# Performance work log

Measured on AMD Instinct MI355X. Metric: run time of the kernel, lower is better.

The kernel has to match this reference:

```python
import jax, jax.numpy as jnp
import numpy as np

# ---- Plane / hashgrid static configuration (matches init_kwargs + gridencoder defaults) ----
LEVEL_DIM = 2
NUM_LEVELS = 16
LOG2_HASHMAP = 19
HASHMAP_MAX = 2 ** LOG2_HASHMAP
BASE_RES = 16               # gridencoder default base_resolution
RESOLUTION = 2048           # desired_resolution
OUTPUT_DIM = 8
HIDDEN_DIM = 64
N_POINTS = 1 << 20
PRIME_Y = np.uint32(2654435761)  # torch-ngp fast_hash prime for dim 1 (dim 0 prime is 1)

# per-level scales / resolutions / table offsets, exactly as in gridencoder
_b = np.exp2(np.log2(RESOLUTION / BASE_RES) / (NUM_LEVELS - 1))
SCALES, RESOLUTIONS, OFFSETS = [], [], [0]
for _l in range(NUM_LEVELS):
    _s = BASE_RES * (_b ** _l) - 1.0
    _r = int(np.ceil(_s)) + 1
    SCALES.append(float(_s)); RESOLUTIONS.append(_r)
    _p = min(HASHMAP_MAX, _r * _r)
    _p = (_p + 7) // 8 * 8  # align to 8 entries
    OFFSETS.append(OFFSETS[-1] + _p)
TOTAL_PARAMS = OFFSETS[-1]


def grid_encode(x, table):
    """Multires 2D hashgrid encoding. x: [N,2] in [0,1], table: [TOTAL_PARAMS, LEVEL_DIM]."""
    feats = []
    for l in range(NUM_LEVELS):
        scale, res = SCALES[l], RESOLUTIONS[l]
        size = OFFSETS[l + 1] - OFFSETS[l]
        pos = x * scale + 0.5                 # [N,2]
        pg = jnp.floor(pos)
        fr = pos - pg                         # bilinear fractions within grid cell
        pg = pg.astype(jnp.uint32)
        acc = jnp.zeros((x.shape[0], LEVEL_DIM), x.dtype)
        for dx in (0, 1):
            for dy in (0, 1):
                gx = pg[:, 0] + jnp.uint32(dx)
                gy = pg[:, 1] + jnp.uint32(dy)
                if res * res > size:
                    # hashed level: fast_hash (xor of prime-multiplied coords) mod table size
                    idx = (gx ^ (gy * PRIME_Y)) % jnp.uint32(size)
                else:
                    # dense level: row-major index, wrapped like the CUDA kernel
                    idx = (gx + gy * jnp.uint32(res)) % jnp.uint32(size)
                wx = fr[:, 0] if dx else 1.0 - fr[:, 0]
                wy = fr[:, 1] if dy else 1.0 - fr[:, 1]
                acc = acc + (wx * wy)[:, None] * table[OFFSETS[l] + idx.astype(jnp.int32)]
        feats.append(acc)
    return jnp.concatenate(feats, axis=-1)  # [N, NUM_LEVELS*LEVEL_DIM] = [N, 32]


def mlp(h, w0, w1):
    # 2-layer bias-free MLP: Linear(32->64) + relu + Linear(64->8)
    return jax.nn.relu(h @ w0.T) @ w1.T


def plane_forward(xy, table, w0, w1, bound):
    xy = (xy + bound) / (2 * bound)
    coords = jnp.clip(xy * RESOLUTION - 0.5, 0, RESOLUTION - 1)
    cx, cy = coords[..., 0], coords[..., 1]
    cx0, cy0 = jnp.floor(cx), jnp.floor(cy)
    cx1 = jnp.clip(cx0 + 1, 0, RESOLUTION - 1)
    cy1 = jnp.clip(cy0 + 1, 0, RESOLUTION - 1)
    u = (cx - cx0)[..., None]
    v = (cy - cy0)[..., None]

    def corner(a, b):
        g = (jnp.stack([a, b], axis=-1) + 0.5) / RESOLUTION
        return mlp(grid_encode(g, table), w0, w1)

    f00 = corner(cx0, cy0)
    f01 = corner(cx0, cy1)
    f10 = corner(cx1, cy0)
    f11 = corner(cx1, cy1)
    return (1 - v) * (1 - u) * f00 + (1 - v) * u * f10 + v * (1 - u) * f01 + v * u * f11


def setup_inputs() -> dict:
    key = jax.random.key(0)
    k1, k2, k3, k4 = jax.random.split(key, 4)
    xy = jax.random.normal(k1, (N_POINTS, 2), jnp.float32)
    table = jax.random.uniform(k2, (TOTAL_PARAMS, LEVEL_DIM), jnp.float32, -1e-4, 1e-4)
    in_dim = NUM_LEVELS * LEVEL_DIM
    w0 = jax.random.normal(k3, (HIDDEN_DIM, in_dim), jnp.float32) * (1.0 / np.sqrt(in_dim))
    w1 = jax.random.normal(k4, (OUTPUT_DIM, HIDDEN_DIM), jnp.float32) * (1.0 / np.sqrt(HIDDEN_DIM))
    return {"xy": xy, "table": table, "w0": w0, "w1": w1, "bound": 1}


def reference(xy, table, w0, w1, bound):
    return plane_forward(xy, table, w0, w1, bound)
```

## Files before the change

### kernel.cpp

```cpp
#include <hip/hip_runtime.h>
#include <math.h>

#define PRIME_Y 2654435761u

struct LevelParams { float scale; unsigned res; unsigned size; unsigned offset; };
struct EncParams { LevelParams lv[16]; };

typedef __attribute__((ext_vector_type(8))) short short8;
typedef __attribute__((ext_vector_type(4))) float f32x4;

struct alignas(8) F2 { float x, y; };

__device__ inline unsigned bf2pack(float a, float b) {
  unsigned r;
  asm("v_cvt_pk_bf16_f32 %0, %1, %2" : "=v"(r) : "v"(a), "v"(b));
  return r;
}
__device__ inline F2 bf2unpack(unsigned u) {
  F2 r;
  r.x = __uint_as_float(u << 16);
  r.y = __uint_as_float(u & 0xFFFF0000u);
  return r;
}

__global__ __launch_bounds__(256) void cvt_table(const F2* __restrict__ in,
                                                 unsigned* __restrict__ outb,
                                                 int n) {
  int i = blockIdx.x * 256 + threadIdx.x;
  if (i < n) {
    F2 v = in[i];
    outb[i] = bf2pack(v.x, v.y);
  }
}

__global__ __launch_bounds__(256) void prep_tables(
    const F2* __restrict__ in, unsigned long long* __restrict__ pair,
    unsigned* __restrict__ packed, EncParams P, unsigned denseTotal,
    unsigned total) {
  unsigned i = blockIdx.x * 256 + threadIdx.x;
  if (i >= total) return;
  F2 a = in[i];
  unsigned pa = bf2pack(a.x, a.y);
  if (i >= denseTotal) { packed[i] = pa; return; }
  unsigned off = 0, size = 0;
  #pragma unroll
  for (int l = 0; l < 12; ++l)
    if (i >= P.lv[l].offset) { off = P.lv[l].offset; size = P.lv[l].size; }
  unsigned j = i - off;
  unsigned j1 = (j + 1u == size) ? 0u : (j + 1u);
  F2 b = in[off + j1];
  pair[i] = ((unsigned long long)bf2pack(b.x, b.y) << 32) | (unsigned long long)pa;
}

#define SMEM_BYTES 39936

template <int TBF>
__global__ __launch_bounds__(256, 4) void plane_fwd(
    const F2* __restrict__ xy,
    const F2* __restrict__ table,
    const unsigned* __restrict__ tbf16,
    const unsigned long long* __restrict__ dpair,
    const float* __restrict__ w0g,
    const float* __restrict__ w1g,
    const int* __restrict__ boundp,
    float* __restrict__ out,
    EncParams P)
{
  __shared__ __align__(16) char smem[SMEM_BYTES];
  const int t = threadIdx.x;
  const int L = t & 63;
  const int w = t >> 6;
  const int r16 = L & 15;
  const int g = L >> 4;

  {
    const float4* s = (const float4*)w0g;
    float4 a = s[t * 2], b = s[t * 2 + 1];
    uint4 pk = make_uint4(bf2pack(a.x, a.y), bf2pack(a.z, a.w),
                          bf2pack(b.x, b.y), bf2pack(b.z, b.w));
    *(uint4*)(smem + (t >> 2) * 80 + (t & 3) * 16) = pk;
  }
  {
    int row = t >> 4;
    int colb = (t & 15) * 8;
    float c0 = 0.f, c1 = 0.f, c2 = 0.f, c3 = 0.f;
    if (row < 8) {
      float4 wv = *(const float4*)(w1g + row * 64 + (t & 15) * 4);
      c0 = wv.x; c1 = wv.y; c2 = wv.z; c3 = wv.w;
    }
    *(uint2*)(smem + 5120 + row * 128 + (colb ^ ((row & 7) << 4))) =
        make_uint2(bf2pack(c0, c1), bf2pack(c2, c3));
  }

  char* sFH = smem + 7168 + w * 8192;

  const int gid = blockIdx.x * 256 + t;
  const int p = gid >> 2;
  const int c = t & 3;
  F2 pxy = xy[p];

  int braw = boundp[0];
  float bf = (braw > 0x00800000) ? __int_as_float(braw) : (float)braw;
  float inv2b = 0.5f / bf;
  float xn = (pxy.x + bf) * inv2b;
  float yn = (pxy.y + bf) * inv2b;

  float cx  = fminf(fmaxf(xn * 2048.0f - 0.5f, 0.0f), 2047.0f);
  float cyv = fminf(fmaxf(yn * 2048.0f - 0.5f, 0.0f), 2047.0f);
  float cx0 = floorf(cx), cy0 = floorf(cyv);
  float u = cx - cx0, v = cyv - cy0;
  float cx1 = fminf(cx0 + 1.0f, 2047.0f);
  float cy1 = fminf(cy0 + 1.0f, 2047.0f);

  const float cxc = (c & 1) ? cx1 : cx0;
  const float cyc = (c & 2) ? cy1 : cy0;
  const float wc = ((c & 1) ? u : 1.0f - u) * ((c & 2) ? v : 1.0f - v);

  const float K = 1.0f / 2048.0f;
  const float gx = (cxc + 0.5f) * K;
  const float gy = (cyc + 0.5f) * K;

  unsigned fw[16];

  if (TBF == 2) {
    unsigned hv[4][4];
    uint2 dv[12][2];

    #pragma unroll
    for (int li = 0; li < 4; ++li) {
      const int l = 12 + li;
      const float scale   = P.lv[l].scale;
      const unsigned size = P.lv[l].size;
      const unsigned off  = P.lv[l].offset;
      float px = fmaf(gx, scale, 0.5f);
      float py = fmaf(gy, scale, 0.5f);
      unsigned ux = (unsigned)floorf(px);
      unsigned uy = (unsigned)floorf(py);
      const unsigned m = size - 1u;
      unsigned hy0 = uy * PRIME_Y;
      unsigned hy1 = hy0 + PRIME_Y;
      const unsigned* tb = tbf16 + off;
      hv[li][0] = tb[(ux ^ hy0) & m];
      hv[li][1] = tb[(ux ^ hy1) & m];
      hv[li][2] = tb[((ux + 1u) ^ hy0) & m];
      hv[li][3] = tb[((ux + 1u) ^ hy1) & m];
    }
    #pragma unroll
    for (int l = 0; l < 12; ++l) {
      const float scale   = P.lv[l].scale;
      const unsigned res  = P.lv[l].res;
      const unsigned size = P.lv[l].size;
      const unsigned off  = P.lv[l].offset;
      float px = fmaf(gx, scale, 0.5f);
      float py = fmaf(gy, scale, 0.5f);
      unsigned ux = (unsigned)floorf(px);
      unsigned uy = (unsigned)floorf(py);
      unsigned v00 = ux + uy * res;
      unsigned v01 = v00 + res;
      v01 = (v01 >= size) ? (v01 - size) : v01;
      const uint2* dp = (const uint2*)(dpair + off);
      dv[l][0] = dp[v00];
      dv[l][1] = dp[v01];
    }

    #pragma unroll
    for (int li = 0; li < 4; ++li) {
      const int l = 12 + li;
      const float scale = P.lv[l].scale;
      float px = fmaf(gx, scale, 0.5f);
      float py = fmaf(gy, scale, 0.5f);
      float frx = px - floorf(px);
      float fry = py - floorf(py);
      F2 t00 = bf2unpack(hv[li][0]);
      F2 t01 = bf2unpack(hv[li][1]);
      F2 t10 = bf2unpack(hv[li][2]);
      F2 t11 = bf2unpack(hv[li][3]);
      float wx0 = 1.0f - frx, wx1 = frx;
      float wy0 = 1.0f - fry, wy1 = fry;
      float w00 = wx0 * wy0, w01 = wx0 * wy1, w10 = wx1 * wy0, w11 = wx1 * wy1;
      float fx = w00 * t00.x + w01 * t01.x + w10 * t10.x + w11 * t11.x;
      float fy = w00 * t00.y + w01 * t01.y + w10 * t10.y + w11 * t11.y;
      fw[l] = bf2pack(fx, fy);
    }
    #pragma unroll
    for (int l = 0; l < 12; ++l) {
      const float scale = P.lv[l].scale;
      float px = fmaf(gx, scale, 0.5f);
      float py = fmaf(gy, scale, 0.5f);
      float frx = px - floorf(px);
      float fry = py - floorf(py);
      F2 t00 = bf2unpack(dv[l][0].x);
      F2 t10 = bf2unpack(dv[l][0].y);
      F2 t01 = bf2unpack(dv[l][1].x);
      F2 t11 = bf2unpack(dv[l][1].y);
      float wx0 = 1.0f - frx, wx1 = frx;
      float wy0 = 1.0f - fry, wy1 = fry;
      float w00 = wx0 * wy0, w01 = wx0 * wy1, w10 = wx1 * wy0, w11 = wx1 * wy1;
      float fx = w00 * t00.x + w01 * t01.x + w10 * t10.x + w11 * t11.x;
      float fy = w00 * t00.y + w01 * t01.y + w10 * t10.y + w11 * t11.y;
      fw[l] = bf2pack(fx, fy);
    }
  } else {
    #pragma unroll
    for (int lidx = 0; lidx < 16; ++lidx) {
      const int l = (lidx < 4) ? (12 + lidx) : (lidx - 4);
      const float scale   = P.lv[l].scale;
      const unsigned res  = P.lv[l].res;
      const unsigned size = P.lv[l].size;
      const unsigned off  = P.lv[l].offset;
      const bool hashed = (res * res) > size;

      float px = fmaf(gx, scale, 0.5f);
      float pgx = floorf(px);
      float frx = px - pgx;
      unsigned ux = (unsigned)pgx;

      float py = fmaf(gy, scale, 0.5f);
      float pgy = floorf(py);
      float fry = py - pgy;
      unsigned uy = (unsigned)pgy;

      unsigned i00, i01, i10, i11;
      if (hashed) {
        const unsigned m = size - 1u;
        unsigned hy0 = uy * PRIME_Y;
        unsigned hy1 = hy0 + PRIME_Y;
        i00 = (ux ^ hy0) & m;
        i01 = (ux ^ hy1) & m;
        i10 = ((ux + 1u) ^ hy0) & m;
        i11 = ((ux + 1u) ^ hy1) & m;
      } else {
        unsigned b0 = uy * res, b1 = b0 + res;
        unsigned q00 = ux + b0,      q01 = ux + b1;
        unsigned q10 = ux + 1u + b0, q11 = ux + 1u + b1;
        i00 = q00 >= size ? q00 - size : q00;
        i01 = q01 >= size ? q01 - size : q01;
        i10 = q10 >= size ? q10 - size : q10;
        i11 = q11 >= size ? q11 - size : q11;
      }

      F2 t00, t01, t10, t11;
      if (TBF == 1) {
        const unsigned* tb = tbf16 + off;
        t00 = bf2unpack(tb[i00]);
        t01 = bf2unpack(tb[i01]);
        t10 = bf2unpack(tb[i10]);
        t11 = bf2unpack(tb[i11]);
      } else {
        const F2* tabp = table + off;
        t00 = tabp[i00]; t01 = tabp[i01]; t10 = tabp[i10]; t11 = tabp[i11];
      }

      float wx0 = 1.0f - frx, wx1 = frx;
      float wy0 = 1.0f - fry, wy1 = fry;
      float w00 = wx0 * wy0, w01 = wx0 * wy1, w10 = wx1 * wy0, w11 = wx1 * wy1;
      float fx = w00 * t00.x + w01 * t01.x + w10 * t10.x + w11 * t11.x;
      float fy = w00 * t00.y + w01 * t01.y + w10 * t10.y + w11 * t11.y;
      fw[l] = bf2pack(fx, fy);
    }
  }

  *(uint4*)(sFH + L * 80 +  0) = make_uint4(fw[0],  fw[1],  fw[2],  fw[3]);
  *(uint4*)(sFH + L * 80 + 16) = make_uint4(fw[4],  fw[5],  fw[6],  fw[7]);
  *(uint4*)(sFH + L * 80 + 32) = make_uint4(fw[8],  fw[9],  fw[10], fw[11]);
  *(uint4*)(sFH + L * 80 + 48) = make_uint4(fw[12], fw[13], fw[14], fw[15]);

  __syncthreads();

  short8 afr[4], bfr[4];
  #pragma unroll
  for (int b = 0; b < 4; ++b)
    bfr[b] = *(const short8*)(sFH + (16 * b + r16) * 80 + g * 16);
  #pragma unroll
  for (int a = 0; a < 4; ++a)
    afr[a] = *(const short8*)(smem + (16 * a + r16) * 80 + g * 16);

  f32x4 acc[4][4];
  #pragma unroll
  for (int a = 0; a < 4; ++a)
    #pragma unroll
    for (int b = 0; b < 4; ++b)
      acc[a][b] = (f32x4){0.f, 0.f, 0.f, 0.f};

  #pragma unroll
  for (int a = 0; a < 4; ++a)
    #pragma unroll
    for (int b = 0; b < 4; ++b)
      acc[a][b] = __builtin_amdgcn_mfma_f32_16x16x32_bf16(
          afr[a], bfr[b], acc[a][b], 0, 0, 0);

  #pragma unroll
  for (int a = 0; a < 4; ++a)
    #pragma unroll
    for (int b = 0; b < 4; ++b) {
      f32x4 h = acc[a][b];
      float h0 = fmaxf(h.x, 0.f), h1 = fmaxf(h.y, 0.f);
      float h2 = fmaxf(h.z, 0.f), h3 = fmaxf(h.w, 0.f);
      *(uint2*)(sFH + (16 * b + r16) * 128 +
                ((a * 32 + g * 8) ^ ((r16 & 7) << 4))) =
          make_uint2(bf2pack(h0, h1), bf2pack(h2, h3));
    }


  f32x4 oacc[4];
  #pragma unroll
  for (int b = 0; b < 4; ++b) oacc[b] = (f32x4){0.f, 0.f, 0.f, 0.f};

  #pragma unroll
  for (int ks = 0; ks < 2; ++ks) {
    short8 a2 = *(const short8*)(smem + 5120 + r16 * 128 +
                                 ((ks * 64 + g * 16) ^ ((r16 & 7) << 4)));
    #pragma unroll
    for (int b = 0; b < 4; ++b) {
      short8 b2 = *(const short8*)(sFH + (16 * b + r16) * 128 +
                                   ((ks * 64 + g * 16) ^ ((r16 & 7) << 4)));
      oacc[b] = __builtin_amdgcn_mfma_f32_16x16x32_bf16(a2, b2, oacc[b], 0, 0, 0);
    }
  }

  #pragma unroll
  for (int b = 0; b < 4; ++b) {
    float wcm = __shfl(wc, 16 * b + r16, 64);
    float v0 = oacc[b].x * wcm;
    float v1 = oacc[b].y * wcm;
    float v2 = oacc[b].z * wcm;
    float v3 = oacc[b].w * wcm;
    v0 += __shfl_xor(v0, 1, 64); v0 += __shfl_xor(v0, 2, 64);
    v1 += __shfl_xor(v1, 1, 64); v1 += __shfl_xor(v1, 2, 64);
    v2 += __shfl_xor(v2, 1, 64); v2 += __shfl_xor(v2, 2, 64);
    v3 += __shfl_xor(v3, 1, 64); v3 += __shfl_xor(v3, 2, 64);
    if ((L & 3) == 0 && g < 2) {
      int pt = blockIdx.x * 64 + w * 16 + 4 * b + (r16 >> 2);
      *(f32x4*)(out + (size_t)pt * 8 + 4 * g) = (f32x4){v0, v1, v2, v3};
    }
  }
}

extern "C" void kernel_launch(void* const* d_in, const int* in_sizes, int n_in,
                              void* d_out, int out_size, void* d_ws, size_t ws_size,
                              hipStream_t stream) {
  EncParams P;
  double b = exp2(log2(2048.0 / 16.0) / 15.0);
  unsigned off = 0;
  for (int l = 0; l < 16; ++l) {
    double s = 16.0 * pow(b, (double)l) - 1.0;
    int r = (int)ceil(s) + 1;
    unsigned p = (unsigned)(r * r);
    if (p > 524288u) p = 524288u;
    p = (p + 7u) / 8u * 8u;
    P.lv[l].scale = (float)s;
    P.lv[l].res = (unsigned)r;
    P.lv[l].size = p;
    P.lv[l].offset = off;
    off += p;
  }
  const int total_params = (int)off;

  int hstart = 16;
  for (int l = 0; l < 16; ++l) {
    unsigned long long rr = (unsigned long long)P.lv[l].res * P.lv[l].res;
    if (rr > P.lv[l].size) { hstart = l; break; }
  }
  const unsigned denseTotal = (hstart < 16) ? P.lv[hstart].offset
                                            : (unsigned)total_params;
  const size_t pairBytes = (size_t)denseTotal * 8;
  const size_t packBytes = (size_t)total_params * 4;

  const int N = in_sizes[0] / 2;
  const F2* xy = (const F2*)d_in[0];
  const F2* table = (const F2*)d_in[1];
  const float* w0g = (const float*)d_in[2];
  const float* w1g = (const float*)d_in[3];
  const int* bp = (const int*)d_in[4];
  float* outp = (float*)d_out;

  if (hstart == 12 && ws_size >= pairBytes + packBytes) {
    unsigned long long* pair = (unsigned long long*)d_ws;
    unsigned* tbf = (unsigned*)((char*)d_ws + pairBytes);
    prep_tables<<<(total_params + 255) / 256, 256, 0, stream>>>(
        table, pair, tbf, P, denseTotal, (unsigned)total_params);
    plane_fwd<2><<<N / 64, 256, 0, stream>>>(xy, table, tbf, pair, w0g, w1g,
                                             bp, outp, P);
  } else if (ws_size >= packBytes) {
    unsigned* tbf = (unsigned*)d_ws;
    cvt_table<<<(total_params + 255) / 256, 256, 0, stream>>>(table, tbf,
                                                              total_params);
    plane_fwd<1><<<N / 64, 256, 0, stream>>>(xy, table, tbf, nullptr, w0g, w1g,
                                             bp, outp, P);
  } else {
    plane_fwd<0><<<N / 64, 256, 0, stream>>>(xy, table, nullptr, nullptr, w0g,
                                             w1g, bp, outp, P);
  }
}
```

Measured before the change: 286.8 us.

## Process all four corners per thread with shared gathers and quad-packed dense tables

```diff
diff --git a/kernel.cpp b/kernel.cpp
--- a/kernel.cpp
+++ b/kernel.cpp
@@ -33,33 +33,39 @@
   }
 }
 
-__global__ __launch_bounds__(256) void prep_tables(
-    const F2* __restrict__ in, unsigned long long* __restrict__ pair,
-    unsigned* __restrict__ packed, EncParams P, unsigned denseTotal,
+__global__ __launch_bounds__(256) void prep3(
+    const F2* __restrict__ in, uint4* __restrict__ quad,
+    unsigned* __restrict__ hp, EncParams P, unsigned denseTotal,
     unsigned total) {
   unsigned i = blockIdx.x * 256 + threadIdx.x;
   if (i >= total) return;
-  F2 a = in[i];
-  unsigned pa = bf2pack(a.x, a.y);
-  if (i >= denseTotal) { packed[i] = pa; return; }
-  unsigned off = 0, size = 0;
+  if (i >= denseTotal) {
+    F2 a = in[i];
+    hp[i - denseTotal] = bf2pack(a.x, a.y);
+    return;
+  }
+  unsigned off = 0, size = 0, res = 0;
   #pragma unroll
   for (int l = 0; l < 12; ++l)
-    if (i >= P.lv[l].offset) { off = P.lv[l].offset; size = P.lv[l].size; }
+    if (i >= P.lv[l].offset) {
+      off = P.lv[l].offset; size = P.lv[l].size; res = P.lv[l].res;
+    }
   unsigned j = i - off;
-  unsigned j1 = (j + 1u == size) ? 0u : (j + 1u);
-  F2 b = in[off + j1];
-  pair[i] = ((unsigned long long)bf2pack(b.x, b.y) << 32) | (unsigned long long)pa;
+  unsigned j1 = j + 1u;        if (j1 >= size) j1 -= size;
+  unsigned j2 = j + res;       if (j2 >= size) j2 -= size;
+  unsigned j3 = j + res + 1u;  if (j3 >= size) j3 -= size;
+  F2 a0 = in[off + j],  a1 = in[off + j1];
+  F2 a2 = in[off + j2], a3 = in[off + j3];
+  quad[i] = make_uint4(bf2pack(a0.x, a0.y), bf2pack(a1.x, a1.y),
+                       bf2pack(a2.x, a2.y), bf2pack(a3.x, a3.y));
 }
 
 #define SMEM_BYTES 39936
 
-template <int TBF>
-__global__ __launch_bounds__(256, 4) void plane_fwd(
+__global__ __launch_bounds__(256, 4) void plane_fwd1(
     const F2* __restrict__ xy,
-    const F2* __restrict__ table,
-    const unsigned* __restrict__ tbf16,
-    const unsigned long long* __restrict__ dpair,
+    const uint4* __restrict__ qtab,
+    const unsigned* __restrict__ hp,
     const float* __restrict__ w0g,
     const float* __restrict__ w1g,
     const int* __restrict__ boundp,
@@ -94,10 +100,8 @@
 
   char* sFH = smem + 7168 + w * 8192;
 
-  const int gid = blockIdx.x * 256 + t;
-  const int p = gid >> 2;
-  const int c = t & 3;
-  F2 pxy = xy[p];
+  const int pt0 = blockIdx.x * 256 + t;
+  F2 pxy = xy[pt0];
 
   int braw = boundp[0];
   float bf = (braw > 0x00800000) ? __int_as_float(braw) : (float)braw;
@@ -112,152 +116,319 @@
   float cx1 = fminf(cx0 + 1.0f, 2047.0f);
   float cy1 = fminf(cy0 + 1.0f, 2047.0f);
 
-  const float cxc = (c & 1) ? cx1 : cx0;
-  const float cyc = (c & 2) ? cy1 : cy0;
-  const float wc = ((c & 1) ? u : 1.0f - u) * ((c & 2) ? v : 1.0f - v);
-
   const float K = 1.0f / 2048.0f;
-  const float gx = (cxc + 0.5f) * K;
-  const float gy = (cyc + 0.5f) * K;
-
-  unsigned fw[16];
-
-  if (TBF == 2) {
-    unsigned hv[4][4];
-    uint2 dv[12][2];
-
-    #pragma unroll
-    for (int li = 0; li < 4; ++li) {
-      const int l = 12 + li;
-      const float scale   = P.lv[l].scale;
-      const unsigned size = P.lv[l].size;
-      const unsigned off  = P.lv[l].offset;
-      float px = fmaf(gx, scale, 0.5f);
-      float py = fmaf(gy, scale, 0.5f);
-      unsigned ux = (unsigned)floorf(px);
-      unsigned uy = (unsigned)floorf(py);
-      const unsigned m = size - 1u;
-      unsigned hy0 = uy * PRIME_Y;
-      unsigned hy1 = hy0 + PRIME_Y;
-      const unsigned* tb = tbf16 + off;
-      hv[li][0] = tb[(ux ^ hy0) & m];
-      hv[li][1] = tb[(ux ^ hy1) & m];
-      hv[li][2] = tb[((ux + 1u) ^ hy0) & m];
-      hv[li][3] = tb[((ux + 1u) ^ hy1) & m];
-    }
-    #pragma unroll
-    for (int l = 0; l < 12; ++l) {
-      const float scale   = P.lv[l].scale;
-      const unsigned res  = P.lv[l].res;
-      const unsigned size = P.lv[l].size;
-      const unsigned off  = P.lv[l].offset;
-      float px = fmaf(gx, scale, 0.5f);
-      float py = fmaf(gy, scale, 0.5f);
-      unsigned ux = (unsigned)floorf(px);
-      unsigned uy = (unsigned)floorf(py);
-      unsigned v00 = ux + uy * res;
-      unsigned v01 = v00 + res;
-      v01 = (v01 >= size) ? (v01 - size) : v01;
-      const uint2* dp = (const uint2*)(dpair + off);
-      dv[l][0] = dp[v00];
-      dv[l][1] = dp[v01];
-    }
-
-    #pragma unroll
-    for (int li = 0; li < 4; ++li) {
-      const int l = 12 + li;
-      const float scale = P.lv[l].scale;
-      float px = fmaf(gx, scale, 0.5f);
-      float py = fmaf(gy, scale, 0.5f);
-      float frx = px - floorf(px);
-      float fry = py - floorf(py);
-      F2 t00 = bf2unpack(hv[li][0]);
-      F2 t01 = bf2unpack(hv[li][1]);
-      F2 t10 = bf2unpack(hv[li][2]);
-      F2 t11 = bf2unpack(hv[li][3]);
+  const float gxc0 = (cx0 + 0.5f) * K, gxc1 = (cx1 + 0.5f) * K;
+  const float gyc0 = (cy0 + 0.5f) * K, gyc1 = (cy1 + 0.5f) * K;
+
+  unsigned fw[4][16];
+  const unsigned denseOff = P.lv[12].offset;
+
+  #pragma unroll
+  for (int li = 0; li < 4; ++li) {
+    const int l = 12 + li;
+    const float scale   = P.lv[l].scale;
+    const unsigned size = P.lv[l].size;
+    const unsigned off  = P.lv[l].offset;
+    const unsigned m = size - 1u;
+    const unsigned* tb = hp + (off - denseOff);
+
+    float px0 = fmaf(gxc0, scale, 0.5f), px1 = fmaf(gxc1, scale, 0.5f);
+    float py0 = fmaf(gyc0, scale, 0.5f), py1 = fmaf(gyc1, scale, 0.5f);
+    float fx0 = floorf(px0), fx1 = floorf(px1);
+    float fy0 = floorf(py0), fy1 = floorf(py1);
+    unsigned ux0 = (unsigned)fx0, ux1 = (unsigned)fx1;
+    unsigned uy0 = (unsigned)fy0, uy1 = (unsigned)fy1;
+    bool xs = (ux1 != ux0), ys = (uy1 != uy0);
+
+    unsigned hy0 = uy0 * PRIME_Y;
+    unsigned hy1 = hy0 + PRIME_Y;
+    unsigned hy2 = hy1 + PRIME_Y;
+
+    unsigned h00 = tb[(ux0 ^ hy0) & m];
+    unsigned h10 = tb[((ux0 + 1u) ^ hy0) & m];
+    unsigned h01 = tb[(ux0 ^ hy1) & m];
+    unsigned h11 = tb[((ux0 + 1u) ^ hy1) & m];
+    unsigned h20 = 0u, h21 = 0u, h02 = 0u, h12 = 0u, h22 = 0u;
+    if (xs)       { h20 = tb[((ux0 + 2u) ^ hy0) & m];
+                    h21 = tb[((ux0 + 2u) ^ hy1) & m]; }
+    if (ys)       { h02 = tb[(ux0 ^ hy2) & m];
+                    h12 = tb[((ux0 + 1u) ^ hy2) & m]; }
+    if (xs && ys) { h22 = tb[((ux0 + 2u) ^ hy2) & m]; }
+
+    float frx0 = px0 - fx0, frx1 = px1 - fx1;
+    float fry0 = py0 - fy0, fry1 = py1 - fy1;
+
+    #pragma unroll
+    for (int c = 0; c < 4; ++c) {
+      const bool cH = (c & 1) != 0, cV = (c & 2) != 0;
+      bool sx = cH && xs, sy = cV && ys;
+      unsigned e00 = sy ? (sx ? h11 : h01) : (sx ? h10 : h00);
+      unsigned e10 = sy ? (sx ? h21 : h11) : (sx ? h20 : h10);
+      unsigned e01 = sy ? (sx ? h12 : h02) : (sx ? h11 : h01);
+      unsigned e11 = sy ? (sx ? h22 : h12) : (sx ? h21 : h11);
+      float frx = cH ? frx1 : frx0;
+      float fry = cV ? fry1 : fry0;
+      F2 t00 = bf2unpack(e00), t10 = bf2unpack(e10);
+      F2 t01 = bf2unpack(e01), t11 = bf2unpack(e11);
       float wx0 = 1.0f - frx, wx1 = frx;
       float wy0 = 1.0f - fry, wy1 = fry;
       float w00 = wx0 * wy0, w01 = wx0 * wy1, w10 = wx1 * wy0, w11 = wx1 * wy1;
       float fx = w00 * t00.x + w01 * t01.x + w10 * t10.x + w11 * t11.x;
       float fy = w00 * t00.y + w01 * t01.y + w10 * t10.y + w11 * t11.y;
-      fw[l] = bf2pack(fx, fy);
-    }
-    #pragma unroll
-    for (int l = 0; l < 12; ++l) {
-      const float scale = P.lv[l].scale;
-      float px = fmaf(gx, scale, 0.5f);
-      float py = fmaf(gy, scale, 0.5f);
-      float frx = px - floorf(px);
-      float fry = py - floorf(py);
-      F2 t00 = bf2unpack(dv[l][0].x);
-      F2 t10 = bf2unpack(dv[l][0].y);
-      F2 t01 = bf2unpack(dv[l][1].x);
-      F2 t11 = bf2unpack(dv[l][1].y);
+      fw[c][l] = bf2pack(fx, fy);
+    }
+  }
+
+  #pragma unroll
+  for (int l = 0; l < 12; ++l) {
+    const float scale   = P.lv[l].scale;
+    const unsigned res  = P.lv[l].res;
+    const unsigned off  = P.lv[l].offset;
+    const uint4* qt = qtab + off;
+
+    float px0 = fmaf(gxc0, scale, 0.5f), px1 = fmaf(gxc1, scale, 0.5f);
+    float py0 = fmaf(gyc0, scale, 0.5f), py1 = fmaf(gyc1, scale, 0.5f);
+    float fx0 = floorf(px0), fx1 = floorf(px1);
+    float fy0 = floorf(py0), fy1 = floorf(py1);
+    unsigned ux0 = (unsigned)fx0, ux1 = (unsigned)fx1;
+    unsigned uy0 = (unsigned)fy0, uy1 = (unsigned)fy1;
+    bool xs = (ux1 != ux0), ys = (uy1 != uy0);
+
+    unsigned vA = ux0 + uy0 * res;
+    uint4 qA = qt[vA];
+    uint4 qB = make_uint4(0u, 0u, 0u, 0u);
+    uint4 qC = make_uint4(0u, 0u, 0u, 0u);
+    uint4 qD = make_uint4(0u, 0u, 0u, 0u);
+    if (xs)       qB = qt[vA + 1u];
+    if (ys)       qC = qt[vA + res];
+    if (xs && ys) qD = qt[vA + res + 1u];
+
+    float frx0 = px0 - fx0, frx1 = px1 - fx1;
+    float fry0 = py0 - fy0, fry1 = py1 - fy1;
+
+    #pragma unroll
+    for (int c = 0; c < 4; ++c) {
+      const bool cH = (c & 1) != 0, cV = (c & 2) != 0;
+      bool sx = cH && xs, sy = cV && ys;
+      unsigned qx = sy ? (sx ? qD.x : qC.x) : (sx ? qB.x : qA.x);
+      unsigned qy = sy ? (sx ? qD.y : qC.y) : (sx ? qB.y : qA.y);
+      unsigned qz = sy ? (sx ? qD.z : qC.z) : (sx ? qB.z : qA.z);
+      unsigned qw = sy ? (sx ? qD.w : qC.w) : (sx ? qB.w : qA.w);
+      float frx = cH ? frx1 : frx0;
+      float fry = cV ? fry1 : fry0;
+      F2 t00 = bf2unpack(qx), t10 = bf2unpack(qy);
+      F2 t01 = bf2unpack(qz), t11 = bf2unpack(qw);
       float wx0 = 1.0f - frx, wx1 = frx;
       float wy0 = 1.0f - fry, wy1 = fry;
       float w00 = wx0 * wy0, w01 = wx0 * wy1, w10 = wx1 * wy0, w11 = wx1 * wy1;
       float fx = w00 * t00.x + w01 * t01.x + w10 * t10.x + w11 * t11.x;
       float fy = w00 * t00.y + w01 * t01.y + w10 * t10.y + w11 * t11.y;
-      fw[l] = bf2pack(fx, fy);
-    }
-  } else {
-    #pragma unroll
-    for (int lidx = 0; lidx < 16; ++lidx) {
-      const int l = (lidx < 4) ? (12 + lidx) : (lidx - 4);
-      const float scale   = P.lv[l].scale;
-      const unsigned res  = P.lv[l].res;
-      const unsigned size = P.lv[l].size;
-      const unsigned off  = P.lv[l].offset;
-      const bool hashed = (res * res) > size;
-
-      float px = fmaf(gx, scale, 0.5f);
-      float pgx = floorf(px);
-      float frx = px - pgx;
-      unsigned ux = (unsigned)pgx;
-
-      float py = fmaf(gy, scale, 0.5f);
-      float pgy = floorf(py);
-      float fry = py - pgy;
-      unsigned uy = (unsigned)pgy;
-
-      unsigned i00, i01, i10, i11;
-      if (hashed) {
-        const unsigned m = size - 1u;
-        unsigned hy0 = uy * PRIME_Y;
-        unsigned hy1 = hy0 + PRIME_Y;
-        i00 = (ux ^ hy0) & m;
-        i01 = (ux ^ hy1) & m;
-        i10 = ((ux + 1u) ^ hy0) & m;
-        i11 = ((ux + 1u) ^ hy1) & m;
-      } else {
-        unsigned b0 = uy * res, b1 = b0 + res;
-        unsigned q00 = ux + b0,      q01 = ux + b1;
-        unsigned q10 = ux + 1u + b0, q11 = ux + 1u + b1;
-        i00 = q00 >= size ? q00 - size : q00;
-        i01 = q01 >= size ? q01 - size : q01;
-        i10 = q10 >= size ? q10 - size : q10;
-        i11 = q11 >= size ? q11 - size : q11;
+      fw[c][l] = bf2pack(fx, fy);
+    }
+  }
+
+  __syncthreads();
+
+  f32x4 outacc[4];
+  #pragma unroll
+  for (int b = 0; b < 4; ++b) outacc[b] = (f32x4){0.f, 0.f, 0.f, 0.f};
+
+  #pragma unroll
+  for (int r = 0; r < 4; ++r) {
+    *(uint4*)(sFH + L * 80 +  0) =
+        make_uint4(fw[r][0],  fw[r][1],  fw[r][2],  fw[r][3]);
+    *(uint4*)(sFH + L * 80 + 16) =
+        make_uint4(fw[r][4],  fw[r][5],  fw[r][6],  fw[r][7]);
+    *(uint4*)(sFH + L * 80 + 32) =
+        make_uint4(fw[r][8],  fw[r][9],  fw[r][10], fw[r][11]);
+    *(uint4*)(sFH + L * 80 + 48) =
+        make_uint4(fw[r][12], fw[r][13], fw[r][14], fw[r][15]);
+
+    short8 bfr[4];
+    #pragma unroll
+    for (int b = 0; b < 4; ++b)
+      bfr[b] = *(const short8*)(sFH + (16 * b + r16) * 80 + g * 16);
+
+    #pragma unroll
+    for (int a = 0; a < 4; ++a) {
+      short8 afr = *(const short8*)(smem + (16 * a + r16) * 80 + g * 16);
+      f32x4 acc[4];
+      #pragma unroll
+      for (int b = 0; b < 4; ++b) acc[b] = (f32x4){0.f, 0.f, 0.f, 0.f};
+      #pragma unroll
+      for (int b = 0; b < 4; ++b)
+        acc[b] = __builtin_amdgcn_mfma_f32_16x16x32_bf16(afr, bfr[b], acc[b],
+                                                         0, 0, 0);
+      #pragma unroll
+      for (int b = 0; b < 4; ++b) {
+        f32x4 h = acc[b];
+        float h0 = fmaxf(h.x, 0.f), h1 = fmaxf(h.y, 0.f);
+        float h2 = fmaxf(h.z, 0.f), h3 = fmaxf(h.w, 0.f);
+        *(uint2*)(sFH + (16 * b + r16) * 128 +
+                  ((a * 32 + g * 8) ^ ((r16 & 7) << 4))) =
+            make_uint2(bf2pack(h0, h1), bf2pack(h2, h3));
       }
-
-      F2 t00, t01, t10, t11;
-      if (TBF == 1) {
-        const unsigned* tb = tbf16 + off;
-        t00 = bf2unpack(tb[i00]);
-        t01 = bf2unpack(tb[i01]);
-        t10 = bf2unpack(tb[i10]);
-        t11 = bf2unpack(tb[i11]);
-      } else {
-        const F2* tabp = table + off;
-        t00 = tabp[i00]; t01 = tabp[i01]; t10 = tabp[i10]; t11 = tabp[i11];
+    }
+
+    f32x4 oacc[4];
+    #pragma unroll
+    for (int b = 0; b < 4; ++b) oacc[b] = (f32x4){0.f, 0.f, 0.f, 0.f};
+    #pragma unroll
+    for (int ks = 0; ks < 2; ++ks) {
+      short8 a2 = *(const short8*)(smem + 5120 + r16 * 128 +
+                                   ((ks * 64 + g * 16) ^ ((r16 & 7) << 4)));
+      #pragma unroll
+      for (int b = 0; b < 4; ++b) {
+        short8 b2 = *(const short8*)(sFH + (16 * b + r16) * 128 +
+                                     ((ks * 64 + g * 16) ^ ((r16 & 7) << 4)));
+        oacc[b] = __builtin_amdgcn_mfma_f32_16x16x32_bf16(a2, b2, oacc[b],
+                                                          0, 0, 0);
       }
-
-      float wx0 = 1.0f - frx, wx1 = frx;
-      float wy0 = 1.0f - fry, wy1 = fry;
-      float w00 = wx0 * wy0, w01 = wx0 * wy1, w10 = wx1 * wy0, w11 = wx1 * wy1;
-      float fx = w00 * t00.x + w01 * t01.x + w10 * t10.x + w11 * t11.x;
-      float fy = w00 * t00.y + w01 * t01.y + w10 * t10.y + w11 * t11.y;
-      fw[l] = bf2pack(fx, fy);
-    }
+    }
+
+    float wcr = ((r & 1) ? u : 1.0f - u) * ((r & 2) ? v : 1.0f - v);
+    #pragma unroll
+    for (int b = 0; b < 4; ++b) {
+      float wcm = __shfl(wcr, 16 * b + r16, 64);
+      outacc[b].x = fmaf(wcm, oacc[b].x, outacc[b].x);
+      outacc[b].y = fmaf(wcm, oacc[b].y, outacc[b].y);
+      outacc[b].z = fmaf(wcm, oacc[b].z, outacc[b].z);
+      outacc[b].w = fmaf(wcm, oacc[b].w, outacc[b].w);
+    }
+  }
+
+  if (g < 2) {
+    #pragma unroll
+    for (int b = 0; b < 4; ++b) {
+      int pt = blockIdx.x * 256 + w * 64 + 16 * b + r16;
+      *(f32x4*)(out + (size_t)pt * 8 + 4 * g) = outacc[b];
+    }
+  }
+}
+
+template <int TBF>
+__global__ __launch_bounds__(256, 4) void plane_fwd(
+    const F2* __restrict__ xy,
+    const F2* __restrict__ table,
+    const unsigned* __restrict__ tbf16,
+    const float* __restrict__ w0g,
+    const float* __restrict__ w1g,
+    const int* __restrict__ boundp,
+    float* __restrict__ out,
+    EncParams P)
+{
+  __shared__ __align__(16) char smem[SMEM_BYTES];
+  const int t = threadIdx.x;
+  const int L = t & 63;
+  const int w = t >> 6;
+  const int r16 = L & 15;
+  const int g = L >> 4;
+
+  {
+    const float4* s = (const float4*)w0g;
+    float4 a = s[t * 2], b = s[t * 2 + 1];
+    uint4 pk = make_uint4(bf2pack(a.x, a.y), bf2pack(a.z, a.w),
+                          bf2pack(b.x, b.y), bf2pack(b.z, b.w));
+    *(uint4*)(smem + (t >> 2) * 80 + (t & 3) * 16) = pk;
+  }
+  {
+    int row = t >> 4;
+    int colb = (t & 15) * 8;
+    float c0 = 0.f, c1 = 0.f, c2 = 0.f, c3 = 0.f;
+    if (row < 8) {
+      float4 wv = *(const float4*)(w1g + row * 64 + (t & 15) * 4);
+      c0 = wv.x; c1 = wv.y; c2 = wv.z; c3 = wv.w;
+    }
+    *(uint2*)(smem + 5120 + row * 128 + (colb ^ ((row & 7) << 4))) =
+        make_uint2(bf2pack(c0, c1), bf2pack(c2, c3));
+  }
+
+  char* sFH = smem + 7168 + w * 8192;
+
+  const int gid = blockIdx.x * 256 + t;
+  const int p = gid >> 2;
+  const int c = t & 3;
+  F2 pxy = xy[p];
+
+  int braw = boundp[0];
+  float bf = (braw > 0x00800000) ? __int_as_float(braw) : (float)braw;
+  float inv2b = 0.5f / bf;
+  float xn = (pxy.x + bf) * inv2b;
+  float yn = (pxy.y + bf) * inv2b;
+
+  float cx  = fminf(fmaxf(xn * 2048.0f - 0.5f, 0.0f), 2047.0f);
+  float cyv = fminf(fmaxf(yn * 2048.0f - 0.5f, 0.0f), 2047.0f);
+  float cx0 = floorf(cx), cy0 = floorf(cyv);
+  float u = cx - cx0, v = cyv - cy0;
+  float cx1 = fminf(cx0 + 1.0f, 2047.0f);
+  float cy1 = fminf(cy0 + 1.0f, 2047.0f);
+
+  const float cxc = (c & 1) ? cx1 : cx0;
+  const float cyc = (c & 2) ? cy1 : cy0;
+  const float wc = ((c & 1) ? u : 1.0f - u) * ((c & 2) ? v : 1.0f - v);
+
+  const float K = 1.0f / 2048.0f;
+  const float gx = (cxc + 0.5f) * K;
+  const float gy = (cyc + 0.5f) * K;
+
+  unsigned fw[16];
+
+  #pragma unroll
+  for (int lidx = 0; lidx < 16; ++lidx) {
+    const int l = (lidx < 4) ? (12 + lidx) : (lidx - 4);
+    const float scale   = P.lv[l].scale;
+    const unsigned res  = P.lv[l].res;
+    const unsigned size = P.lv[l].size;
+    const unsigned off  = P.lv[l].offset;
+    const bool hashed = (res * res) > size;
+
+    float px = fmaf(gx, scale, 0.5f);
+    float pgx = floorf(px);
+    float frx = px - pgx;
+    unsigned ux = (unsigned)pgx;
+
+    float py = fmaf(gy, scale, 0.5f);
+    float pgy = floorf(py);
+    float fry = py - pgy;
+    unsigned uy = (unsigned)pgy;
+
+    unsigned i00, i01, i10, i11;
+    if (hashed) {
+      const unsigned m = size - 1u;
+      unsigned hy0 = uy * PRIME_Y;
+      unsigned hy1 = hy0 + PRIME_Y;
+      i00 = (ux ^ hy0) & m;
+      i01 = (ux ^ hy1) & m;
+      i10 = ((ux + 1u) ^ hy0) & m;
+      i11 = ((ux + 1u) ^ hy1) & m;
+    } else {
+      unsigned b0 = uy * res, b1 = b0 + res;
+      unsigned q00 = ux + b0,      q01 = ux + b1;
+      unsigned q10 = ux + 1u + b0, q11 = ux + 1u + b1;
+      i00 = q00 >= size ? q00 - size : q00;
+      i01 = q01 >= size ? q01 - size : q01;
+      i10 = q10 >= size ? q10 - size : q10;
+      i11 = q11 >= size ? q11 - size : q11;
+    }
+
+    F2 t00, t01, t10, t11;
+    if (TBF == 1) {
+      const unsigned* tb = tbf16 + off;
+      t00 = bf2unpack(tb[i00]);
+      t01 = bf2unpack(tb[i01]);
+      t10 = bf2unpack(tb[i10]);
+      t11 = bf2unpack(tb[i11]);
+    } else {
+      const F2* tabp = table + off;
+      t00 = tabp[i00]; t01 = tabp[i01]; t10 = tabp[i10]; t11 = tabp[i11];
+    }
+
+    float wx0 = 1.0f - frx, wx1 = frx;
+    float wy0 = 1.0f - fry, wy1 = fry;
+    float w00 = wx0 * wy0, w01 = wx0 * wy1, w10 = wx1 * wy0, w11 = wx1 * wy1;
+    float fx = w00 * t00.x + w01 * t01.x + w10 * t10.x + w11 * t11.x;
+    float fy = w00 * t00.y + w01 * t01.y + w10 * t10.y + w11 * t11.y;
+    fw[l] = bf2pack(fx, fy);
   }
 
   *(uint4*)(sFH + L * 80 +  0) = make_uint4(fw[0],  fw[1],  fw[2],  fw[3]);
@@ -300,7 +471,6 @@
                 ((a * 32 + g * 8) ^ ((r16 & 7) << 4))) =
           make_uint2(bf2pack(h0, h1), bf2pack(h2, h3));
     }
-
 
   f32x4 oacc[4];
   #pragma unroll
@@ -363,7 +533,8 @@
   }
   const unsigned denseTotal = (hstart < 16) ? P.lv[hstart].offset
                                             : (unsigned)total_params;
-  const size_t pairBytes = (size_t)denseTotal * 8;
+  const size_t quadBytes = (size_t)denseTotal * 16;
+  const size_t hashBytes = (size_t)((unsigned)total_params - denseTotal) * 4;
   const size_t packBytes = (size_t)total_params * 4;
 
   const int N = in_sizes[0] / 2;
@@ -374,21 +545,21 @@
   const int* bp = (const int*)d_in[4];
   float* outp = (float*)d_out;
 
-  if (hstart == 12 && ws_size >= pairBytes + packBytes) {
-    unsigned long long* pair = (unsigned long long*)d_ws;
-    unsigned* tbf = (unsigned*)((char*)d_ws + pairBytes);
-    prep_tables<<<(total_params + 255) / 256, 256, 0, stream>>>(
-        table, pair, tbf, P, denseTotal, (unsigned)total_params);
-    plane_fwd<2><<<N / 64, 256, 0, stream>>>(xy, table, tbf, pair, w0g, w1g,
-                                             bp, outp, P);
+  if (hstart == 12 && (N & 255) == 0 && ws_size >= quadBytes + hashBytes) {
+    uint4* quad = (uint4*)d_ws;
+    unsigned* hp = (unsigned*)((char*)d_ws + quadBytes);
+    prep3<<<(total_params + 255) / 256, 256, 0, stream>>>(
+        table, quad, hp, P, denseTotal, (unsigned)total_params);
+    plane_fwd1<<<N / 256, 256, 0, stream>>>(xy, quad, hp, w0g, w1g, bp,
+                                            outp, P);
   } else if (ws_size >= packBytes) {
     unsigned* tbf = (unsigned*)d_ws;
     cvt_table<<<(total_params + 255) / 256, 256, 0, stream>>>(table, tbf,
                                                               total_params);
-    plane_fwd<1><<<N / 64, 256, 0, stream>>>(xy, table, tbf, nullptr, w0g, w1g,
-                                             bp, outp, P);
+    plane_fwd<1><<<N / 64, 256, 0, stream>>>(xy, table, tbf, w0g, w1g, bp,
+                                             outp, P);
   } else {
-    plane_fwd<0><<<N / 64, 256, 0, stream>>>(xy, table, nullptr, nullptr, w0g,
-                                             w1g, bp, outp, P);
-  }
-}
+    plane_fwd<0><<<N / 64, 256, 0, stream>>>(xy, table, nullptr, w0g, w1g, bp,
+                                             outp, P);
+  }
+}
```

New measurement: 248.4 us. -13.4%, faster.
